# Optimization experiments

Hardware: AMD Instinct MI355X
Metric: run time of the kernel (lower is better)

The kernel has to match this reference:

```python
import jax, jax.numpy as jnp
import numpy as np

B, L, D = 4, 4096, 1024
H, W = 16, 64          # n_heads, window_size
HD = D // H            # head_dim
EPS = 1e-5


def setup_inputs() -> dict:
    key = jax.random.key(0)
    ks = jax.random.split(key, 3)
    s = 1.0 / np.sqrt(D)
    x = jax.random.normal(ks[0], (B, L, D), dtype=jnp.float32)
    Wqkv = (jax.random.normal(ks[1], (3 * D, D), dtype=jnp.float32) * s)
    bqkv = jnp.zeros((3 * D,), dtype=jnp.float32)
    Wproj = (jax.random.normal(ks[2], (D, D), dtype=jnp.float32) * s)
    bproj = jnp.zeros((D,), dtype=jnp.float32)
    gamma = jnp.ones((D,), dtype=jnp.float32)
    beta = jnp.zeros((D,), dtype=jnp.float32)
    return {"x": x, "Wqkv": Wqkv, "bqkv": bqkv, "Wproj": Wproj,
            "bproj": bproj, "gamma": gamma, "beta": beta}


def reference(x, Wqkv, bqkv, Wproj, bproj, gamma, beta):
    scale = HD ** -0.5
    nw = L // W  # L is a multiple of W, so pad_len == 0 (same math as padded path)
    # QKV projection -> [3, B, H, L, HD]
    qkv = (x @ Wqkv.T + bqkv).reshape(B, L, 3, H, HD).transpose(2, 0, 3, 1, 4)
    q, k, v = qkv[0], qkv[1], qkv[2]
    # split into non-overlapping windows: [B, H, nw, W, HD]
    q = q.reshape(B, H, nw, W, HD)
    k = k.reshape(B, H, nw, W, HD)
    v = v.reshape(B, H, nw, W, HD)
    attn = jax.nn.softmax(jnp.einsum('bhnqd,bhnkd->bhnqk', q, k) * scale, axis=-1)
    out = jnp.einsum('bhnqk,bhnkd->bhnqd', attn, v)  # dropout is identity in eval
    out = out.reshape(B, H, L, HD).transpose(0, 2, 1, 3).reshape(B, L, D)
    out = out @ Wproj.T + bproj
    y = out + x
    mean = jnp.mean(y, axis=-1, keepdims=True)
    var = jnp.mean((y - mean) ** 2, axis=-1, keepdims=True)
    return (y - mean) * jax.lax.rsqrt(var + EPS) * gamma + beta
```

## Files before the change

### kernel.cpp

```cpp
#include <hip/hip_runtime.h>
#include <stdint.h>


typedef __attribute__((ext_vector_type(8))) short short8;
typedef __attribute__((ext_vector_type(4))) float float4v;
typedef unsigned short us;

#define GAS const __attribute__((address_space(1))) void
#define LAS __attribute__((address_space(3))) void

__device__ __forceinline__ float bf2f(us u) {
  return __uint_as_float(((unsigned int)u) << 16);
}
__device__ __forceinline__ us f2bf(float f) {
  unsigned int u = __float_as_uint(f);
  unsigned int r = u + 0x7FFFu + ((u >> 16) & 1u);
  return (us)(r >> 16);
}
__device__ __forceinline__ int4 stage8(const float* p) {
  float4 a = *(const float4*)p;
  float4 b = *(const float4*)(p + 4);
  int4 r;
  us* u = (us*)&r;
  u[0] = f2bf(a.x); u[1] = f2bf(a.y); u[2] = f2bf(a.z); u[3] = f2bf(a.w);
  u[4] = f2bf(b.x); u[5] = f2bf(b.y); u[6] = f2bf(b.z); u[7] = f2bf(b.w);
  return r;
}
__device__ __forceinline__ int4 stage8(const us* p) { return *(const int4*)p; }
__device__ __forceinline__ void stc(us* p, float v) { *p = f2bf(v); }
__device__ __forceinline__ void stc(float* p, float v) { *p = v; }

__global__ __launch_bounds__(256) void cast_bf16(const float* __restrict__ src,
                                                 us* __restrict__ dst, int n8) {
  const int i = blockIdx.x * 256 + threadIdx.x;
  if (i < n8) *(int4*)(dst + (size_t)i * 8) = stage8(src + (size_t)i * 8);
}

template <int N, int K, int EPI, int HM, typename CT>
__global__ __launch_bounds__(512, 1) void gemm256(
    const us* __restrict__ A, const us* __restrict__ Bt,
    const float* __restrict__ bias, const float* __restrict__ resid,
    CT* __restrict__ C) {
  constexpr int NBX = N / 256;
  constexpr int NWG = NBX * 64;
  __shared__ __align__(16) us As[2][256 * 64];
  __shared__ __align__(16) us Bs[2][256 * 64];
  const int tid = threadIdx.x;
  const int lane = tid & 63;
  const int wave = tid >> 6;
  const int wm = wave >> 2;
  const int wn = wave & 3;
  const int lr = lane & 15, lq = lane >> 4;

  int id = blockIdx.y * NBX + blockIdx.x;
  id = (id & 7) * (NWG / 8) + (id >> 3);
  const int m0 = (id / NBX) * 256;
  const int n0 = (id % NBX) * 256;

  const int trow = tid >> 3;
  const int tcol = (((tid & 7) ^ (trow & 7)) * 8);

  constexpr int NT = K / 64;

  float4v acc[8][4];
#pragma unroll
  for (int i = 0; i < 8; i++)
#pragma unroll
    for (int j = 0; j < 4; j++) acc[i][j] = (float4v)0.0f;

#define STAGE256(buf, t)                                                       \
  do {                                                                         \
    const size_t kof = (size_t)(t) * 64;                                       \
    _Pragma("unroll") for (int q = 0; q < 4; q++) {                            \
      const us* ga = A + (size_t)(m0 + q * 64 + trow) * K + kof + tcol;        \
      __builtin_amdgcn_global_load_lds((GAS*)ga,                               \
          (LAS*)&As[buf][(q * 512 + tid) * 8], 16, 0, 0);                      \
    }                                                                          \
    _Pragma("unroll") for (int q = 0; q < 4; q++) {                            \
      const us* gb = Bt + (size_t)(n0 + q * 64 + trow) * K + kof + tcol;       \
      __builtin_amdgcn_global_load_lds((GAS*)gb,                               \
          (LAS*)&Bs[buf][(q * 512 + tid) * 8], 16, 0, 0);                      \
    }                                                                          \
  } while (0)

  STAGE256(0, 0);

  for (int t = 0; t < NT; t++) {
    const int cur = t & 1;
    __builtin_amdgcn_s_barrier();
    if (t + 1 < NT) {
      STAGE256(cur ^ 1, t + 1);
      asm volatile("s_waitcnt vmcnt(8)" ::: "memory");
    } else {
      asm volatile("s_waitcnt vmcnt(0)" ::: "memory");
    }
    __builtin_amdgcn_s_barrier();

    const us* Ab = As[cur];
    const us* Bb = Bs[cur];
#pragma unroll
    for (int kk8 = 0; kk8 < 2; kk8++) {
      short8 bf8[4];
#pragma unroll
      for (int nt = 0; nt < 4; nt++) {
        const int row = wn * 64 + nt * 16 + lr;
        bf8[nt] = *(const short8*)&Bb[row * 64 + (((kk8 * 4 + lq) ^ (lr & 7)) * 8)];
      }
#pragma unroll
      for (int mh = 0; mh < 2; mh++) {
        short8 af[4];
#pragma unroll
        for (int mt = 0; mt < 4; mt++) {
          const int row = wm * 128 + mh * 64 + mt * 16 + lr;
          af[mt] = *(const short8*)&Ab[row * 64 + (((kk8 * 4 + lq) ^ (lr & 7)) * 8)];
        }
        __builtin_amdgcn_s_setprio(1);
#pragma unroll
        for (int mt = 0; mt < 4; mt++)
#pragma unroll
          for (int nt = 0; nt < 4; nt++)
            acc[mh * 4 + mt][nt] = __builtin_amdgcn_mfma_f32_16x16x32_bf16(
                af[mt], bf8[nt], acc[mh * 4 + mt][nt], 0, 0, 0);
        __builtin_amdgcn_s_setprio(0);
      }
    }
  }
#undef STAGE256

  float bb[4];
#pragma unroll
  for (int nt = 0; nt < 4; nt++) bb[nt] = bias[n0 + wn * 64 + nt * 16 + lr];
#pragma unroll
  for (int mh = 0; mh < 2; mh++)
#pragma unroll
    for (int mt = 0; mt < 4; mt++) {
      const int rbase = m0 + wm * 128 + mh * 64 + mt * 16 + lq * 4;
#pragma unroll
      for (int nt = 0; nt < 4; nt++) {
        const int col = n0 + wn * 64 + nt * 16 + lr;
#pragma unroll
        for (int r = 0; r < 4; r++) {
          float v = acc[mh * 4 + mt][nt][r] + bb[nt];
          const int row = rbase + r;
          size_t idx;
          if (HM) {
            const int mat = col >> 10, hh = (col >> 6) & 15, d = col & 63;
            idx = (size_t)mat * (16384u * 1024u) +
                  (size_t)((row >> 12) * 16 + hh) * (4096u * 64u) +
                  (size_t)(row & 4095) * 64 + d;
          } else {
            idx = (size_t)row * N + col;
          }
          if (EPI) v += resid[idx];
          stc(&C[idx], v);
        }
      }
    }
}

__global__ __launch_bounds__(256) void attn_mfma(
    const us* __restrict__ qkv, us* __restrict__ attn) {
  __shared__ __align__(16) us Vt[64 * 64];
  __shared__ __align__(16) us Pl[4 * 16 * 64];
  const int wid = blockIdx.x;
  const int wi = wid & 63;
  const int h = (wid >> 6) & 15;
  const int b = wid >> 10;
  const int tid = threadIdx.x;
  const int lane = tid & 63;
  const int w = tid >> 6;
  const int lr = lane & 15, lq = lane >> 4;
  const int rowbase = b * 4096 + wi * 64;

  const us* Qb = qkv + (size_t)(b * 16 + h) * (4096u * 64u) + (size_t)wi * 4096;
  const us* Kb = Qb + (size_t)16384 * 1024;
  const us* Vb = Kb + (size_t)16384 * 1024;

  {
    const int r = lane;
    const int cs = w * 16;
    const us* vsrc = Vb + (size_t)r * 64 + cs;
    int4 v0 = *(const int4*)vsrc;
    int4 v1 = *(const int4*)(vsrc + 8);
    const us* vv0 = (const us*)&v0;
    const us* vv1 = (const us*)&v1;
#pragma unroll
    for (int i = 0; i < 8; i++) {
      const int d = cs + i;
      Vt[d * 64 + (((r >> 3) ^ (d & 7)) * 8) + (r & 7)] = vv0[i];
    }
#pragma unroll
    for (int i = 0; i < 8; i++) {
      const int d = cs + 8 + i;
      Vt[d * 64 + (((r >> 3) ^ (d & 7)) * 8) + (r & 7)] = vv1[i];
    }
  }

  short8 aq[2];
  {
    const us* qrow = Qb + (size_t)(w * 16 + lr) * 64 + lq * 8;
    aq[0] = *(const short8*)qrow;
    aq[1] = *(const short8*)(qrow + 32);
  }
  float4v s[4];
#pragma unroll
  for (int nt = 0; nt < 4; nt++) s[nt] = (float4v)0.0f;
#pragma unroll
  for (int kk8 = 0; kk8 < 2; kk8++) {
#pragma unroll
    for (int nt = 0; nt < 4; nt++) {
      const us* krow = Kb + (size_t)(nt * 16 + lr) * 64 + kk8 * 32 + lq * 8;
      short8 bk = *(const short8*)krow;
      s[nt] = __builtin_amdgcn_mfma_f32_16x16x32_bf16(aq[kk8], bk, s[nt], 0, 0, 0);
    }
  }

  float p[4][4];
#pragma unroll
  for (int r = 0; r < 4; r++) {
    float mx = -1e30f;
#pragma unroll
    for (int nt = 0; nt < 4; nt++) {
      s[nt][r] *= 0.125f;
      mx = fmaxf(mx, s[nt][r]);
    }
    mx = fmaxf(mx, __shfl_xor(mx, 1));
    mx = fmaxf(mx, __shfl_xor(mx, 2));
    mx = fmaxf(mx, __shfl_xor(mx, 4));
    mx = fmaxf(mx, __shfl_xor(mx, 8));
    float sum = 0.f;
#pragma unroll
    for (int nt = 0; nt < 4; nt++) {
      p[nt][r] = __expf(s[nt][r] - mx);
      sum += p[nt][r];
    }
    sum += __shfl_xor(sum, 1);
    sum += __shfl_xor(sum, 2);
    sum += __shfl_xor(sum, 4);
    sum += __shfl_xor(sum, 8);
    const float inv = 1.0f / sum;
#pragma unroll
    for (int nt = 0; nt < 4; nt++) p[nt][r] *= inv;
  }

  us* pw = Pl + w * 1024;
#pragma unroll
  for (int nt = 0; nt < 4; nt++) {
    const int c = nt * 16 + lr;
#pragma unroll
    for (int r = 0; r < 4; r++) {
      const int row = lq * 4 + r;
      pw[row * 64 + (((c >> 3) ^ (row & 7)) * 8) + (c & 7)] = f2bf(p[nt][r]);
    }
  }
  __syncthreads();

  float4v o[4];
#pragma unroll
  for (int nt = 0; nt < 4; nt++) o[nt] = (float4v)0.0f;
#pragma unroll
  for (int kk8 = 0; kk8 < 2; kk8++) {
    short8 pa = *(const short8*)&pw[lr * 64 + (((lq + kk8 * 4) ^ (lr & 7)) * 8)];
#pragma unroll
    for (int nt = 0; nt < 4; nt++) {
      const int d = nt * 16 + lr;
      short8 vb = *(const short8*)&Vt[d * 64 + (((lq + kk8 * 4) ^ (d & 7)) * 8)];
      o[nt] = __builtin_amdgcn_mfma_f32_16x16x32_bf16(pa, vb, o[nt], 0, 0, 0);
    }
  }

#pragma unroll
  for (int nt = 0; nt < 4; nt++) {
    const int c = nt * 16 + lr;
#pragma unroll
    for (int r = 0; r < 4; r++) {
      const int row = lq * 4 + r;
      pw[row * 64 + (((c >> 3) ^ (row & 7)) * 8) + (c & 7)] = f2bf(o[nt][r]);
    }
  }
  {
    const int row = lr;
    const int g0 = ((lq * 2) ^ (row & 7)) * 8;
    const int g1 = ((lq * 2 + 1) ^ (row & 7)) * 8;
    int4 v0 = *(const int4*)&pw[row * 64 + g0];
    int4 v1 = *(const int4*)&pw[row * 64 + g1];
    us* dst = attn + (size_t)(rowbase + w * 16 + row) * 1024 + h * 64 + lq * 16;
    *(int4*)dst = v0;
    *(int4*)(dst + 8) = v1;
  }
}

template <int N, int K, int EPI, typename AT, typename CT>
__global__ __launch_bounds__(256) void gemm_bt(
    const AT* __restrict__ A, const float* __restrict__ Bt,
    const float* __restrict__ bias, const float* __restrict__ resid,
    CT* __restrict__ C) {
  __shared__ __align__(16) us As[128 * 64];
  __shared__ __align__(16) us Bs[128 * 64];
  const int tid = threadIdx.x;
  const int lane = tid & 63;
  const int wave = tid >> 6;
  const int wm = wave >> 1, wn = wave & 1;
  const int lr = lane & 15, lq = lane >> 4;
  const int m0 = blockIdx.y * 128;
  const int n0 = blockIdx.x * 128;
  const int trow = tid >> 3;
  const int tcol = (tid & 7) * 8;

  float4v acc[4][4];
#pragma unroll
  for (int i = 0; i < 4; i++)
#pragma unroll
    for (int j = 0; j < 4; j++) acc[i][j] = (float4v)0.0f;

  for (int k0 = 0; k0 < K; k0 += 64) {
    int4 av[4], bv[4];
#pragma unroll
    for (int p = 0; p < 4; p++) {
      av[p] = stage8(A + (size_t)(m0 + p * 32 + trow) * K + k0 + tcol);
      bv[p] = stage8(Bt + (size_t)(n0 + p * 32 + trow) * K + k0 + tcol);
    }
#pragma unroll
    for (int p = 0; p < 4; p++) {
      *(int4*)&As[(p * 256 + tid) * 8] = av[p];
      *(int4*)&Bs[(p * 256 + tid) * 8] = bv[p];
    }
    __syncthreads();
#pragma unroll
    for (int kk = 0; kk < 64; kk += 32) {
      short8 af[4], bfv[4];
#pragma unroll
      for (int mt = 0; mt < 4; mt++)
        af[mt] = *(const short8*)&As[(wm * 64 + mt * 16 + lr) * 64 + kk + lq * 8];
#pragma unroll
      for (int nt = 0; nt < 4; nt++)
        bfv[nt] = *(const short8*)&Bs[(wn * 64 + nt * 16 + lr) * 64 + kk + lq * 8];
#pragma unroll
      for (int mt = 0; mt < 4; mt++)
#pragma unroll
        for (int nt = 0; nt < 4; nt++)
          acc[mt][nt] = __builtin_amdgcn_mfma_f32_16x16x32_bf16(
              af[mt], bfv[nt], acc[mt][nt], 0, 0, 0);
    }
    __syncthreads();
  }

  float bb[4];
#pragma unroll
  for (int nt = 0; nt < 4; nt++) bb[nt] = bias[n0 + wn * 64 + nt * 16 + lr];
#pragma unroll
  for (int mt = 0; mt < 4; mt++) {
    const int rbase = m0 + wm * 64 + mt * 16 + lq * 4;
#pragma unroll
    for (int nt = 0; nt < 4; nt++) {
      const int col = n0 + wn * 64 + nt * 16 + lr;
#pragma unroll
      for (int r = 0; r < 4; r++) {
        float v = acc[mt][nt][r] + bb[nt];
        size_t idx = (size_t)(rbase + r) * N + col;
        if (EPI) v += resid[idx];
        stc(&C[idx], v);
      }
    }
  }
}

__global__ __launch_bounds__(256) void attn_win(
    const us* __restrict__ qkv, us* __restrict__ attn) {
  __shared__ float qs[64][65];
  __shared__ float ks[64][65];
  __shared__ float vs[64][65];
  const int wid = blockIdx.x;
  const int wi = wid & 63;
  const int h = (wid >> 6) & 15;
  const int b = wid >> 10;
  const int t = threadIdx.x;
  const int rowbase = b * 4096 + wi * 64;
  {
    const int r = t >> 2;
    const int cs = (t & 3) * 16;
    const us* base = qkv + (size_t)(rowbase + r) * 3072 + h * 64 + cs;
#pragma unroll
    for (int s = 0; s < 3; s++) {
      float* dst = (s == 0) ? &qs[r][cs] : (s == 1) ? &ks[r][cs] : &vs[r][cs];
      const us* src = base + s * 1024;
#pragma unroll
      for (int half = 0; half < 2; half++) {
        int4 dv = *(const int4*)(src + half * 8);
        const us* tp = (const us*)&dv;
#pragma unroll
        for (int i = 0; i < 8; i++) dst[half * 8 + i] = bf2f(tp[i]);
      }
    }
  }
  __syncthreads();
  const int r0 = (t >> 4) * 4;
  const int c0 = (t & 15) * 4;
  float acc[4][4] = {};
#pragma unroll 8
  for (int k = 0; k < 64; k++) {
    float qv[4], kv[4];
#pragma unroll
    for (int i = 0; i < 4; i++) qv[i] = qs[r0 + i][k];
#pragma unroll
    for (int j = 0; j < 4; j++) kv[j] = ks[c0 + j][k];
#pragma unroll
    for (int i = 0; i < 4; i++)
#pragma unroll
      for (int j = 0; j < 4; j++) acc[i][j] += qv[i] * kv[j];
  }
  __syncthreads();
#pragma unroll
  for (int i = 0; i < 4; i++)
#pragma unroll
    for (int j = 0; j < 4; j++) qs[r0 + i][c0 + j] = acc[i][j] * 0.125f;
  __syncthreads();
  {
    const int rr = t >> 2;
    const int cs = (t & 3) * 16;
    float pv[16];
    float m = -1e30f;
#pragma unroll
    for (int i = 0; i < 16; i++) {
      pv[i] = qs[rr][cs + i];
      m = fmaxf(m, pv[i]);
    }
    m = fmaxf(m, __shfl_xor(m, 1));
    m = fmaxf(m, __shfl_xor(m, 2));
    float ssum = 0.f;
#pragma unroll
    for (int i = 0; i < 16; i++) {
      pv[i] = __expf(pv[i] - m);
      ssum += pv[i];
    }
    ssum += __shfl_xor(ssum, 1);
    ssum += __shfl_xor(ssum, 2);
    const float inv = 1.0f / ssum;
#pragma unroll
    for (int i = 0; i < 16; i++) qs[rr][cs + i] = pv[i] * inv;
  }
  __syncthreads();
  float o[4][4] = {};
#pragma unroll 8
  for (int k = 0; k < 64; k++) {
    float pr[4], vv[4];
#pragma unroll
    for (int i = 0; i < 4; i++) pr[i] = qs[r0 + i][k];
#pragma unroll
    for (int j = 0; j < 4; j++) vv[j] = vs[k][c0 + j];
#pragma unroll
    for (int i = 0; i < 4; i++)
#pragma unroll
      for (int j = 0; j < 4; j++) o[i][j] += pr[i] * vv[j];
  }
#pragma unroll
  for (int i = 0; i < 4; i++)
#pragma unroll
    for (int j = 0; j < 4; j++)
      attn[(size_t)(rowbase + r0 + i) * 1024 + h * 64 + c0 + j] = f2bf(o[i][j]);
}

__global__ __launch_bounds__(256) void ln_wave(
    float* __restrict__ y, const float* __restrict__ gamma,
    const float* __restrict__ beta) {
  const int row = blockIdx.x * 4 + (threadIdx.x >> 6);
  const int lane = threadIdx.x & 63;
  float* yr = y + (size_t)row * 1024;
  float4 v[4];
  float s1 = 0.f, s2 = 0.f;
#pragma unroll
  for (int i = 0; i < 4; i++) {
    v[i] = *(const float4*)(yr + (i * 64 + lane) * 4);
    s1 += v[i].x + v[i].y + v[i].z + v[i].w;
    s2 += v[i].x * v[i].x + v[i].y * v[i].y + v[i].z * v[i].z + v[i].w * v[i].w;
  }
#pragma unroll
  for (int off = 32; off > 0; off >>= 1) {
    s1 += __shfl_xor(s1, off);
    s2 += __shfl_xor(s2, off);
  }
  const float mean = s1 * (1.0f / 1024.0f);
  const float var = s2 * (1.0f / 1024.0f) - mean * mean;
  const float rstd = rsqrtf(var + 1e-5f);
#pragma unroll
  for (int i = 0; i < 4; i++) {
    float4 g = *(const float4*)(gamma + (i * 64 + lane) * 4);
    float4 bt = *(const float4*)(beta + (i * 64 + lane) * 4);
    float4 o;
    o.x = (v[i].x - mean) * rstd * g.x + bt.x;
    o.y = (v[i].y - mean) * rstd * g.y + bt.y;
    o.z = (v[i].z - mean) * rstd * g.z + bt.z;
    o.w = (v[i].w - mean) * rstd * g.w + bt.w;
    *(float4*)(yr + (i * 64 + lane) * 4) = o;
  }
}

extern "C" void kernel_launch(void* const* d_in, const int* in_sizes, int n_in,
                              void* d_out, int out_size, void* d_ws,
                              size_t ws_size, hipStream_t stream) {
  const float* x = (const float*)d_in[0];
  const float* Wqkv = (const float*)d_in[1];
  const float* bqkv = (const float*)d_in[2];
  const float* Wproj = (const float*)d_in[3];
  const float* bproj = (const float*)d_in[4];
  const float* gamma = (const float*)d_in[5];
  const float* beta = (const float*)d_in[6];
  float* out = (float*)d_out;

  us* qkv = (us*)d_ws;
  us* attn = qkv + (size_t)16384 * 3072;
  us* xb = attn + (size_t)16384 * 1024;
  us* Wqkvb = xb + (size_t)16384 * 1024;
  us* Wprojb = Wqkvb + (size_t)3072 * 1024;
  const size_t need =
      ((size_t)16384 * 3072 + 3 * (size_t)16384 * 1024 + (size_t)3072 * 1024 +
       (size_t)1024 * 1024) * sizeof(us);

  if (ws_size >= need) {
    cast_bf16<<<(16384 * 1024 / 8 + 255) / 256, 256, 0, stream>>>(x, xb,
                                                                  16384 * 128);
    cast_bf16<<<(3072 * 1024 / 8 + 255) / 256, 256, 0, stream>>>(Wqkv, Wqkvb,
                                                                 3072 * 128);
    cast_bf16<<<(1024 * 1024 / 8 + 255) / 256, 256, 0, stream>>>(Wproj, Wprojb,
                                                                 1024 * 128);
    gemm256<3072, 1024, 0, 1, us><<<dim3(12, 64), 512, 0, stream>>>(
        xb, Wqkvb, bqkv, nullptr, qkv);
    attn_mfma<<<4096, 256, 0, stream>>>(qkv, attn);
    gemm256<1024, 1024, 1, 0, float><<<dim3(4, 64), 512, 0, stream>>>(
        attn, Wprojb, bproj, x, out);
  } else {
    gemm_bt<3072, 1024, 0, float, us><<<dim3(24, 128), 256, 0, stream>>>(
        x, Wqkv, bqkv, nullptr, qkv);
    attn_win<<<4096, 256, 0, stream>>>(qkv, attn);
    gemm_bt<1024, 1024, 1, us, float><<<dim3(8, 128), 256, 0, stream>>>(
        attn, Wproj, bproj, x, out);
  }
  ln_wave<<<4096, 256, 0, stream>>>(out, gamma, beta);
}
```

Measured before the change: 345.1 us.

## Stage GEMM epilogue through LDS for coalesced stores and merge cast kernels

The GEMM epilogue now writes accumulators into a padded LDS tile (reusing the staging buffers) and then stores rows with vectorized float4/packed bf16 writes, with vectorized residual loads. Previously each lane did scattered scalar stores. The three bf16 cast launches are merged into one kernel to save launch overhead. The attention block index mapping is also permuted, changing the order in which batch, head and window are visited, likely for cache locality. The cost is extra LDS traffic and barriers in the epilogue, and a larger static shared allocation.

```diff
diff --git a/kernel.cpp b/kernel.cpp
--- a/kernel.cpp
+++ b/kernel.cpp
@@ -30,10 +30,22 @@
 __device__ __forceinline__ void stc(us* p, float v) { *p = f2bf(v); }
 __device__ __forceinline__ void stc(float* p, float v) { *p = v; }
 
-__global__ __launch_bounds__(256) void cast_bf16(const float* __restrict__ src,
-                                                 us* __restrict__ dst, int n8) {
+__global__ __launch_bounds__(256) void cast_all(
+    const float* __restrict__ x, const float* __restrict__ wq,
+    const float* __restrict__ wp, us* __restrict__ xb, us* __restrict__ wqb,
+    us* __restrict__ wpb) {
   const int i = blockIdx.x * 256 + threadIdx.x;
-  if (i < n8) *(int4*)(dst + (size_t)i * 8) = stage8(src + (size_t)i * 8);
+  constexpr int n1 = 16384 * 128;
+  constexpr int n2 = 3072 * 128;
+  if (i < n1) {
+    *(int4*)(xb + (size_t)i * 8) = stage8(x + (size_t)i * 8);
+  } else if (i < n1 + n2) {
+    const int j = i - n1;
+    *(int4*)(wqb + (size_t)j * 8) = stage8(wq + (size_t)j * 8);
+  } else {
+    const int j = i - n1 - n2;
+    *(int4*)(wpb + (size_t)j * 8) = stage8(wp + (size_t)j * 8);
+  }
 }
 
 template <int N, int K, int EPI, int HM, typename CT>
@@ -43,8 +55,10 @@
     CT* __restrict__ C) {
   constexpr int NBX = N / 256;
   constexpr int NWG = NBX * 64;
-  __shared__ __align__(16) us As[2][256 * 64];
-  __shared__ __align__(16) us Bs[2][256 * 64];
+  __shared__ __align__(16) unsigned char RAW[133120];
+  us* AsB = (us*)RAW;
+  us* BsB = (us*)(RAW + 65536);
+  float* EPIF = (float*)RAW;
   const int tid = threadIdx.x;
   const int lane = tid & 63;
   const int wave = tid >> 6;
@@ -74,12 +88,12 @@
     _Pragma("unroll") for (int q = 0; q < 4; q++) {                            \
       const us* ga = A + (size_t)(m0 + q * 64 + trow) * K + kof + tcol;        \
       __builtin_amdgcn_global_load_lds((GAS*)ga,                               \
-          (LAS*)&As[buf][(q * 512 + tid) * 8], 16, 0, 0);                      \
+          (LAS*)&AsB[(buf)*16384 + (q * 512 + tid) * 8], 16, 0, 0);            \
     }                                                                          \
     _Pragma("unroll") for (int q = 0; q < 4; q++) {                            \
       const us* gb = Bt + (size_t)(n0 + q * 64 + trow) * K + kof + tcol;       \
       __builtin_amdgcn_global_load_lds((GAS*)gb,                               \
-          (LAS*)&Bs[buf][(q * 512 + tid) * 8], 16, 0, 0);                      \
+          (LAS*)&BsB[(buf)*16384 + (q * 512 + tid) * 8], 16, 0, 0);            \
     }                                                                          \
   } while (0)
 
@@ -96,8 +110,8 @@
     }
     __builtin_amdgcn_s_barrier();
 
-    const us* Ab = As[cur];
-    const us* Bb = Bs[cur];
+    const us* Ab = AsB + cur * 16384;
+    const us* Bb = BsB + cur * 16384;
 #pragma unroll
     for (int kk8 = 0; kk8 < 2; kk8++) {
       short8 bf8[4];
@@ -130,32 +144,50 @@
   float bb[4];
 #pragma unroll
   for (int nt = 0; nt < 4; nt++) bb[nt] = bias[n0 + wn * 64 + nt * 16 + lr];
-#pragma unroll
-  for (int mh = 0; mh < 2; mh++)
+
+#pragma unroll
+  for (int p = 0; p < 2; p++) {
+    __builtin_amdgcn_s_barrier();
 #pragma unroll
     for (int mt = 0; mt < 4; mt++) {
-      const int rbase = m0 + wm * 128 + mh * 64 + mt * 16 + lq * 4;
+      const int cr = wm * 64 + mt * 16 + lq * 4;
 #pragma unroll
       for (int nt = 0; nt < 4; nt++) {
-        const int col = n0 + wn * 64 + nt * 16 + lr;
-#pragma unroll
-        for (int r = 0; r < 4; r++) {
-          float v = acc[mh * 4 + mt][nt][r] + bb[nt];
-          const int row = rbase + r;
-          size_t idx;
-          if (HM) {
-            const int mat = col >> 10, hh = (col >> 6) & 15, d = col & 63;
-            idx = (size_t)mat * (16384u * 1024u) +
-                  (size_t)((row >> 12) * 16 + hh) * (4096u * 64u) +
-                  (size_t)(row & 4095) * 64 + d;
-          } else {
-            idx = (size_t)row * N + col;
-          }
-          if (EPI) v += resid[idx];
-          stc(&C[idx], v);
-        }
-      }
-    }
+        const int ccol = wn * 64 + nt * 16 + lr;
+#pragma unroll
+        for (int r = 0; r < 4; r++)
+          EPIF[(cr + r) * 260 + ccol] = acc[p * 4 + mt][nt][r] + bb[nt];
+      }
+    }
+    __builtin_amdgcn_s_barrier();
+    const int rr = tid >> 2, cq = tid & 3;
+    const int grow = m0 + (rr >> 6) * 128 + p * 64 + (rr & 63);
+#pragma unroll
+    for (int i = 0; i < 16; i++) {
+      const int ii = (i + cq * 4) & 15;
+      float4 v = *(const float4*)&EPIF[rr * 260 + cq * 64 + ii * 4];
+      const int gcol = n0 + cq * 64 + ii * 4;
+      size_t idx;
+      if (HM) {
+        const int mat = gcol >> 10, hh = (gcol >> 6) & 15, d = gcol & 63;
+        idx = (size_t)mat * (16384u * 1024u) +
+              (size_t)((grow >> 12) * 16 + hh) * (4096u * 64u) +
+              (size_t)(grow & 4095) * 64 + d;
+      } else {
+        idx = (size_t)grow * N + gcol;
+      }
+      if (EPI) {
+        const float4 rv = *(const float4*)&resid[idx];
+        v.x += rv.x; v.y += rv.y; v.z += rv.z; v.w += rv.w;
+      }
+      if constexpr (sizeof(CT) == 2) {
+        us pk[4] = {f2bf(v.x), f2bf(v.y), f2bf(v.z), f2bf(v.w)};
+        *(int2*)&C[idx] = *(int2*)pk;
+      } else {
+        *(float4*)&C[idx] = *(float4*)&v;
+      }
+    }
+  }
 }
 
 __global__ __launch_bounds__(256) void attn_mfma(
@@ -163,9 +195,11 @@
   __shared__ __align__(16) us Vt[64 * 64];
   __shared__ __align__(16) us Pl[4 * 16 * 64];
   const int wid = blockIdx.x;
-  const int wi = wid & 63;
-  const int h = (wid >> 6) & 15;
-  const int b = wid >> 10;
+  const int x = wid & 7;
+  const int k = wid >> 3;
+  const int b = x >> 1;
+  const int h = k >> 5;
+  const int wi = ((x & 1) << 5) | (k & 31);
   const int tid = threadIdx.x;
   const int lane = tid & 63;
   const int w = tid >> 6;
@@ -517,12 +551,9 @@
        (size_t)1024 * 1024) * sizeof(us);
 
   if (ws_size >= need) {
-    cast_bf16<<<(16384 * 1024 / 8 + 255) / 256, 256, 0, stream>>>(x, xb,
-                                                                  16384 * 128);
-    cast_bf16<<<(3072 * 1024 / 8 + 255) / 256, 256, 0, stream>>>(Wqkv, Wqkvb,
-                                                                 3072 * 128);
-    cast_bf16<<<(1024 * 1024 / 8 + 255) / 256, 256, 0, stream>>>(Wproj, Wprojb,
-                                                                 1024 * 128);
+    constexpr int ncast = 16384 * 128 + 3072 * 128 + 1024 * 128;
+    cast_all<<<ncast / 256, 256, 0, stream>>>(x, Wqkv, Wproj, xb, Wqkvb,
+                                              Wprojb);
     gemm256<3072, 1024, 0, 1, us><<<dim3(12, 64), 512, 0, stream>>>(
         xb, Wqkvb, bqkv, nullptr, qkv);
     attn_mfma<<<4096, 256, 0, stream>>>(qkv, attn);
```

Result: slower. 384.6 us (+11.4%).
